# Optimization experiments

Measured on AMD Instinct MI355X. Metric: run time of the kernel, lower is better.

The kernel has to match this reference:

```python
import jax, jax.numpy as jnp
import numpy as np

N_NODES = 100000
N_EDGES = 1600000
HID = 128


def setup_inputs() -> dict:
    key = jax.random.key(0)
    ks = jax.random.split(key, 9)
    return {
        "x": jax.random.normal(ks[0], (N_NODES, 3), dtype=jnp.float32),
        "edge_index": jax.random.randint(ks[1], (2, N_EDGES), 0, N_NODES, dtype=jnp.int64),
        "W_lift": jax.random.normal(ks[2], (3, HID), dtype=jnp.float32) * 0.1,
        "b_lift": jax.random.normal(ks[3], (HID,), dtype=jnp.float32) * 0.1,
        "W_rel": jax.random.normal(ks[4], (HID, HID), dtype=jnp.float32) * 0.05,
        "b_rel": jax.random.normal(ks[5], (HID,), dtype=jnp.float32) * 0.05,
        "W_root": jax.random.normal(ks[6], (HID, HID), dtype=jnp.float32) * 0.05,
        "W_proj": jax.random.normal(ks[7], (HID, 1), dtype=jnp.float32) * 0.1,
        "b_proj": jax.random.normal(ks[8], (1,), dtype=jnp.float32) * 0.1,
    }


def reference(x, edge_index, W_lift, b_lift, W_rel, b_rel, W_root, W_proj, b_proj):
    # Lifting: [N, 3] -> [N, 128]
    h = x @ W_lift + b_lift
    # GraphConv (PyG): out_i = lin_rel(sum_{j in N(i)} h_j) + lin_root(h_i)
    src, dst = edge_index[0], edge_index[1]
    # gather neighbor features then scatter-add to targets
    agg = jax.ops.segment_sum(h[src], dst, num_segments=N_NODES)  # [N, 128]
    h = agg @ W_rel + b_rel + h @ W_root
    h = jnp.tanh(h)
    # Projection: [N, 128] -> [N, 1]
    return h @ W_proj + b_proj
```

## Files before the change

kernel.cpp:

```cpp
#include <hip/hip_runtime.h>
#include <stdint.h>

#define NN 100000
#define NE 1600000
#define HID 128

#define PSCALE 512.0f
#define PINV   (1.0f / 512.0f)
#define PBIAS  8.0f
#define FMASK  0x7FFFFULL

#define NBINS 391
#define CAP   5120
#define NB3   391
#define TB3   512
#define EB    4096

__device__ __forceinline__ void prep_weights(
    const float* __restrict__ W_lift, const float* __restrict__ b_lift,
    const float* __restrict__ W_rel, const float* __restrict__ b_rel,
    const float* __restrict__ W_root, float* __restrict__ Wf) {
    int t = threadIdx.x;
    if (t >= HID) return;
    float lr0 = 0.f, lr1 = 0.f, lr2 = 0.f;
    float xr0 = 0.f, xr1 = 0.f, xr2 = 0.f;
    float blr = 0.f, bxr = 0.f;
    for (int k = 0; k < HID; ++k) {
        float wr = W_rel[k * HID + t];
        float wo = W_root[k * HID + t];
        float bl = b_lift[k];
        float a0 = W_lift[0 * HID + k];
        float a1 = W_lift[1 * HID + k];
        float a2 = W_lift[2 * HID + k];
        lr0 += a0 * wr; lr1 += a1 * wr; lr2 += a2 * wr;
        xr0 += a0 * wo; xr1 += a1 * wo; xr2 += a2 * wo;
        blr += bl * wr; bxr += bl * wo;
    }
    Wf[0 * HID + t] = lr0;
    Wf[1 * HID + t] = lr1;
    Wf[2 * HID + t] = lr2;
    Wf[3 * HID + t] = xr0;
    Wf[4 * HID + t] = xr1;
    Wf[5 * HID + t] = xr2;
    Wf[6 * HID + t] = blr;
    Wf[7 * HID + t] = b_rel[t] + bxr;
}

__device__ __forceinline__ unsigned long long pack_edge(const float* __restrict__ x, int s) {
    float x0 = x[3 * s + 0];
    float x1 = x[3 * s + 1];
    float x2 = x[3 * s + 2];
    unsigned long long u0 = (unsigned)__float2int_rn((x0 + PBIAS) * PSCALE);
    unsigned long long u1 = (unsigned)__float2int_rn((x1 + PBIAS) * PSCALE);
    unsigned long long u2 = (unsigned)__float2int_rn((x2 + PBIAS) * PSCALE);
    return u0 | (u1 << 19) | (u2 << 38) | (1ULL << 57);
}

__global__ __launch_bounds__(TB3) void radix_scatter_prep(
    const int* __restrict__ edges,
    const float* __restrict__ x,
    unsigned* __restrict__ galloc,
    ulonglong2* __restrict__ records,
    const float* __restrict__ W_lift,
    const float* __restrict__ b_lift,
    const float* __restrict__ W_rel,
    const float* __restrict__ b_rel,
    const float* __restrict__ W_root,
    float* __restrict__ Wf) {
    if (blockIdx.x == NB3) {
        prep_weights(W_lift, b_lift, W_rel, b_rel, W_root, Wf);
        return;
    }
    __shared__ unsigned hist[NBINS];
    __shared__ unsigned base[NBINS];
    for (int j = threadIdx.x; j < NBINS; j += TB3) hist[j] = 0;
    __syncthreads();

    const int e0 = blockIdx.x * EB;
    for (int k = 0; k < EB; k += TB3) {
        int e = e0 + k + threadIdx.x;
        if (e >= NE) break;
        int d = edges[NE + e];
        if ((unsigned)d < NN) atomicAdd(&hist[d >> 8], 1u);
    }
    __syncthreads();
    for (int j = threadIdx.x; j < NBINS; j += TB3) {
        unsigned c = hist[j];
        base[j] = c ? atomicAdd(&galloc[j], c) : 0u;
        hist[j] = 0;
    }
    __syncthreads();
    for (int k = 0; k < EB; k += TB3) {
        int e = e0 + k + threadIdx.x;
        if (e >= NE) break;
        int s = edges[e];
        int d = edges[NE + e];
        if ((unsigned)s >= NN || (unsigned)d >= NN) continue;
        unsigned long long pk = pack_edge(x, s);
        int b = d >> 8;
        unsigned pos = base[b] + atomicAdd(&hist[b], 1u);
        if (pos < CAP)
            records[(size_t)b * CAP + pos] = make_ulonglong2((unsigned long long)d, pk);
    }
}

__global__ __launch_bounds__(256) void accum_node_kernel(
    const unsigned* __restrict__ galloc,
    const ulonglong2* __restrict__ records,
    const float* __restrict__ x,
    const float* __restrict__ Wf,
    const float* __restrict__ W_proj,
    const float* __restrict__ b_proj,
    float* __restrict__ out) {
    __shared__ unsigned long long acc[256];
    __shared__ float sWt[HID][8];
    __shared__ float sP[HID];
    acc[threadIdx.x] = 0ULL;
    for (int j = threadIdx.x; j < 8 * HID; j += blockDim.x) {
        int r = j >> 7;
        int t = j & (HID - 1);
        sWt[t][r] = Wf[j];
    }
    for (int j = threadIdx.x; j < HID; j += blockDim.x) sP[j] = W_proj[j];
    __syncthreads();

    const int b = blockIdx.x;
    unsigned cnt = galloc[b];
    if (cnt > CAP) cnt = CAP;
    const ulonglong2* rec = records + (size_t)b * CAP;
    for (unsigned i = threadIdx.x; i < cnt; i += 256) {
        ulonglong2 r = rec[i];
        atomicAdd(&acc[(unsigned)r.x & 255u], r.y);
    }
    __syncthreads();

    int node = b * 256 + threadIdx.x;
    if (node >= NN) return;

    unsigned long long p = acc[threadIdx.x];
    float degf = (float)(unsigned)(p >> 57);
    float a0 = (float)(unsigned)(p & FMASK) * PINV - PBIAS * degf;
    float a1 = (float)(unsigned)((p >> 19) & FMASK) * PINV - PBIAS * degf;
    float a2 = (float)(unsigned)((p >> 38) & FMASK) * PINV - PBIAS * degf;

    float x0 = x[3 * node + 0];
    float x1 = x[3 * node + 1];
    float x2 = x[3 * node + 2];

    float s = 0.f;
#pragma unroll 8
    for (int t = 0; t < HID; ++t) {
        float4 A = *(const float4*)&sWt[t][0];
        float4 B = *(const float4*)&sWt[t][4];
        float h = B.w
                + a0 * A.x + a1 * A.y + a2 * A.z
                + x0 * A.w + x1 * B.x + x2 * B.y
                + degf * B.z;
        float th = 1.f - 2.f / (__expf(2.f * h) + 1.f);
        s += th * sP[t];
    }
    out[node] = s + b_proj[0];
}

__global__ __launch_bounds__(256) void scatter_prep_kernel(
    const int* __restrict__ edges,
    const float* __restrict__ x,
    unsigned long long* __restrict__ aggp,
    const float* __restrict__ W_lift,
    const float* __restrict__ b_lift,
    const float* __restrict__ W_rel,
    const float* __restrict__ b_rel,
    const float* __restrict__ W_root,
    float* __restrict__ Wf) {
    if (blockIdx.x == 0) {
        prep_weights(W_lift, b_lift, W_rel, b_rel, W_root, Wf);
        return;
    }
    int e = (blockIdx.x - 1) * blockDim.x + threadIdx.x;
    if (e >= NE) return;
    int s = edges[e];
    int d = edges[NE + e];
    if ((unsigned)s >= NN || (unsigned)d >= NN) return;
    atomicAdd(&aggp[d], pack_edge(x, s));
}

__global__ __launch_bounds__(256) void node_kernel(
    const float* __restrict__ x,
    const unsigned long long* __restrict__ aggp,
    const float* __restrict__ Wf,
    const float* __restrict__ W_proj,
    const float* __restrict__ b_proj,
    float* __restrict__ out) {
    __shared__ float sWt[HID][8];
    __shared__ float sP[HID];
    for (int j = threadIdx.x; j < 8 * HID; j += blockDim.x) {
        int r = j >> 7;
        int t = j & (HID - 1);
        sWt[t][r] = Wf[j];
    }
    for (int j = threadIdx.x; j < HID; j += blockDim.x) sP[j] = W_proj[j];
    __syncthreads();

    int i = blockIdx.x * blockDim.x + threadIdx.x;
    if (i >= NN) return;

    unsigned long long p = aggp[i];
    float degf = (float)(unsigned)(p >> 57);
    float a0 = (float)(unsigned)(p & FMASK) * PINV - PBIAS * degf;
    float a1 = (float)(unsigned)((p >> 19) & FMASK) * PINV - PBIAS * degf;
    float a2 = (float)(unsigned)((p >> 38) & FMASK) * PINV - PBIAS * degf;

    float x0 = x[3 * i + 0];
    float x1 = x[3 * i + 1];
    float x2 = x[3 * i + 2];

    float acc = 0.f;
#pragma unroll 8
    for (int t = 0; t < HID; ++t) {
        float4 A = *(const float4*)&sWt[t][0];
        float4 B = *(const float4*)&sWt[t][4];
        float h = B.w
                + a0 * A.x + a1 * A.y + a2 * A.z
                + x0 * A.w + x1 * B.x + x2 * B.y
                + degf * B.z;
        float th = 1.f - 2.f / (__expf(2.f * h) + 1.f);
        acc += th * sP[t];
    }
    out[i] = acc + b_proj[0];
}

extern "C" void kernel_launch(void* const* d_in, const int* in_sizes, int n_in,
                              void* d_out, int out_size, void* d_ws, size_t ws_size,
                              hipStream_t stream) {
    const float* x      = (const float*)d_in[0];
    const int*   edges  = (const int*)d_in[1];
    const float* W_lift = (const float*)d_in[2];
    const float* b_lift = (const float*)d_in[3];
    const float* W_rel  = (const float*)d_in[4];
    const float* b_rel  = (const float*)d_in[5];
    const float* W_root = (const float*)d_in[6];
    const float* W_proj = (const float*)d_in[7];
    const float* b_proj = (const float*)d_in[8];
    float* out = (float*)d_out;

    const size_t off_rec = 4096;
    const size_t off_wf  = off_rec + (size_t)NBINS * CAP * 16;
    const size_t needed  = off_wf + 8 * HID * sizeof(float);

    if (ws_size >= needed) {
        unsigned* galloc = (unsigned*)d_ws;
        ulonglong2* records = (ulonglong2*)((char*)d_ws + off_rec);
        float* Wf = (float*)((char*)d_ws + off_wf);

        hipMemsetAsync(galloc, 0, NBINS * sizeof(unsigned), stream);
        radix_scatter_prep<<<NB3 + 1, TB3, 0, stream>>>(
            edges, x, galloc, records, W_lift, b_lift, W_rel, b_rel, W_root, Wf);
        accum_node_kernel<<<NBINS, 256, 0, stream>>>(
            galloc, records, x, Wf, W_proj, b_proj, out);
    } else {
        unsigned long long* aggp = (unsigned long long*)d_ws;
        float* Wf = (float*)((char*)d_ws + (size_t)NN * 8);
        hipMemsetAsync(aggp, 0, (size_t)NN * 8, stream);
        scatter_prep_kernel<<<1 + (NE + 255) / 256, 256, 0, stream>>>(
            edges, x, aggp, W_lift, b_lift, W_rel, b_rel, W_root, Wf);
        node_kernel<<<(NN + 255) / 256, 256, 0, stream>>>(
            x, aggp, Wf, W_proj, b_proj, out);
    }
}
```

Measured before the change: 145.8 us.

## Compact edge records to 8 bytes and shard bin allocators per XCD

Edge records shrink from 16 to 8 bytes by storing only the low destination byte and three 13-bit quantized coordinates, which are re-expanded into the packed accumulator format in the accumulate kernel. Each bin's global allocation counter and record region is split into eight slices indexed by the hardware XCC id, meant to cut cross-die atomic contention and keep record writes local. Edge indices are now loaded once into registers and reused across the histogram and scatter passes instead of being re-read. Clamping to 13 bits narrows the representable range, and each slice's capacity of 1280 risks overflow, which silently drops edges if XCC assignment is uneven.

```diff
diff --git a/kernel.cpp b/kernel.cpp
--- a/kernel.cpp
+++ b/kernel.cpp
@@ -11,10 +11,18 @@
 #define FMASK  0x7FFFFULL
 
 #define NBINS 391
-#define CAP   5120
+#define NSLC  8
+#define SCAP  1280
 #define NB3   391
 #define TB3   512
 #define EB    4096
+#define EPT   (EB / TB3)
+
+__device__ __forceinline__ unsigned xcc_id() {
+    unsigned x;
+    asm volatile("s_getreg_b32 %0, hwreg(HW_REG_XCC_ID)" : "=s"(x));
+    return x & (NSLC - 1);
+}
 
 __device__ __forceinline__ void prep_weights(
     const float* __restrict__ W_lift, const float* __restrict__ b_lift,
@@ -46,21 +54,11 @@
     Wf[7 * HID + t] = b_rel[t] + bxr;
 }
 
-__device__ __forceinline__ unsigned long long pack_edge(const float* __restrict__ x, int s) {
-    float x0 = x[3 * s + 0];
-    float x1 = x[3 * s + 1];
-    float x2 = x[3 * s + 2];
-    unsigned long long u0 = (unsigned)__float2int_rn((x0 + PBIAS) * PSCALE);
-    unsigned long long u1 = (unsigned)__float2int_rn((x1 + PBIAS) * PSCALE);
-    unsigned long long u2 = (unsigned)__float2int_rn((x2 + PBIAS) * PSCALE);
-    return u0 | (u1 << 19) | (u2 << 38) | (1ULL << 57);
-}
-
 __global__ __launch_bounds__(TB3) void radix_scatter_prep(
     const int* __restrict__ edges,
     const float* __restrict__ x,
     unsigned* __restrict__ galloc,
-    ulonglong2* __restrict__ records,
+    unsigned long long* __restrict__ records,
     const float* __restrict__ W_lift,
     const float* __restrict__ b_lift,
     const float* __restrict__ W_rel,
@@ -76,37 +74,52 @@
     for (int j = threadIdx.x; j < NBINS; j += TB3) hist[j] = 0;
     __syncthreads();
 
+    const unsigned myxcd = xcc_id();
     const int e0 = blockIdx.x * EB;
-    for (int k = 0; k < EB; k += TB3) {
-        int e = e0 + k + threadIdx.x;
-        if (e >= NE) break;
-        int d = edges[NE + e];
-        if ((unsigned)d < NN) atomicAdd(&hist[d >> 8], 1u);
+
+    int sreg[EPT], dreg[EPT];
+#pragma unroll
+    for (int k = 0; k < EPT; ++k) {
+        int e = e0 + k * TB3 + threadIdx.x;
+        int s = (e < NE) ? edges[e] : -1;
+        int d = (e < NE) ? edges[NE + e] : -1;
+        bool ok = ((unsigned)s < NN) && ((unsigned)d < NN);
+        sreg[k] = ok ? s : -1;
+        dreg[k] = ok ? d : -1;
+        if (ok) atomicAdd(&hist[d >> 8], 1u);
     }
     __syncthreads();
     for (int j = threadIdx.x; j < NBINS; j += TB3) {
         unsigned c = hist[j];
-        base[j] = c ? atomicAdd(&galloc[j], c) : 0u;
+        base[j] = c ? atomicAdd(&galloc[j * NSLC + myxcd], c) : 0u;
         hist[j] = 0;
     }
     __syncthreads();
-    for (int k = 0; k < EB; k += TB3) {
-        int e = e0 + k + threadIdx.x;
-        if (e >= NE) break;
-        int s = edges[e];
-        int d = edges[NE + e];
-        if ((unsigned)s >= NN || (unsigned)d >= NN) continue;
-        unsigned long long pk = pack_edge(x, s);
+#pragma unroll
+    for (int k = 0; k < EPT; ++k) {
+        int d = dreg[k];
+        if (d < 0) continue;
+        int s = sreg[k];
+        float x0 = x[3 * s + 0];
+        float x1 = x[3 * s + 1];
+        float x2 = x[3 * s + 2];
+        unsigned u0 = min((unsigned)__float2int_rn((x0 + PBIAS) * PSCALE), 8191u);
+        unsigned u1 = min((unsigned)__float2int_rn((x1 + PBIAS) * PSCALE), 8191u);
+        unsigned u2 = min((unsigned)__float2int_rn((x2 + PBIAS) * PSCALE), 8191u);
+        unsigned long long r = (unsigned long long)(d & 255)
+                             | ((unsigned long long)u0 << 8)
+                             | ((unsigned long long)u1 << 21)
+                             | ((unsigned long long)u2 << 34);
         int b = d >> 8;
         unsigned pos = base[b] + atomicAdd(&hist[b], 1u);
-        if (pos < CAP)
-            records[(size_t)b * CAP + pos] = make_ulonglong2((unsigned long long)d, pk);
+        if (pos < SCAP)
+            records[((size_t)b * NSLC + myxcd) * SCAP + pos] = r;
     }
 }
 
 __global__ __launch_bounds__(256) void accum_node_kernel(
     const unsigned* __restrict__ galloc,
-    const ulonglong2* __restrict__ records,
+    const unsigned long long* __restrict__ records,
     const float* __restrict__ x,
     const float* __restrict__ Wf,
     const float* __restrict__ W_proj,
@@ -125,12 +138,19 @@
     __syncthreads();
 
     const int b = blockIdx.x;
-    unsigned cnt = galloc[b];
-    if (cnt > CAP) cnt = CAP;
-    const ulonglong2* rec = records + (size_t)b * CAP;
-    for (unsigned i = threadIdx.x; i < cnt; i += 256) {
-        ulonglong2 r = rec[i];
-        atomicAdd(&acc[(unsigned)r.x & 255u], r.y);
+#pragma unroll
+    for (int sl = 0; sl < NSLC; ++sl) {
+        unsigned cnt = galloc[b * NSLC + sl];
+        if (cnt > SCAP) cnt = SCAP;
+        const unsigned long long* rec = records + ((size_t)b * NSLC + sl) * SCAP;
+        for (unsigned i = threadIdx.x; i < cnt; i += 256) {
+            unsigned long long r = rec[i];
+            unsigned long long add = ((r >> 8)  & 0x1FFFULL)
+                                   | (((r >> 21) & 0x1FFFULL) << 19)
+                                   | (((r >> 34) & 0x1FFFULL) << 38)
+                                   | (1ULL << 57);
+            atomicAdd(&acc[(unsigned)r & 255u], add);
+        }
     }
     __syncthreads();
 
@@ -181,7 +201,13 @@
     int s = edges[e];
     int d = edges[NE + e];
     if ((unsigned)s >= NN || (unsigned)d >= NN) return;
-    atomicAdd(&aggp[d], pack_edge(x, s));
+    float x0 = x[3 * s + 0];
+    float x1 = x[3 * s + 1];
+    float x2 = x[3 * s + 2];
+    unsigned long long u0 = (unsigned)__float2int_rn((x0 + PBIAS) * PSCALE);
+    unsigned long long u1 = (unsigned)__float2int_rn((x1 + PBIAS) * PSCALE);
+    unsigned long long u2 = (unsigned)__float2int_rn((x2 + PBIAS) * PSCALE);
+    atomicAdd(&aggp[d], u0 | (u1 << 19) | (u2 << 38) | (1ULL << 57));
 }
 
 __global__ __launch_bounds__(256) void node_kernel(
@@ -243,16 +269,16 @@
     const float* b_proj = (const float*)d_in[8];
     float* out = (float*)d_out;
 
-    const size_t off_rec = 4096;
-    const size_t off_wf  = off_rec + (size_t)NBINS * CAP * 16;
+    const size_t off_rec = 16384;
+    const size_t off_wf  = off_rec + (size_t)NBINS * NSLC * SCAP * 8;
     const size_t needed  = off_wf + 8 * HID * sizeof(float);
 
     if (ws_size >= needed) {
         unsigned* galloc = (unsigned*)d_ws;
-        ulonglong2* records = (ulonglong2*)((char*)d_ws + off_rec);
+        unsigned long long* records = (unsigned long long*)((char*)d_ws + off_rec);
         float* Wf = (float*)((char*)d_ws + off_wf);
 
-        hipMemsetAsync(galloc, 0, NBINS * sizeof(unsigned), stream);
+        hipMemsetAsync(galloc, 0, NBINS * NSLC * sizeof(unsigned), stream);
         radix_scatter_prep<<<NB3 + 1, TB3, 0, stream>>>(
             edges, x, galloc, records, W_lift, b_lift, W_rel, b_rel, W_root, Wf);
         accum_node_kernel<<<NBINS, 256, 0, stream>>>(
```

New measurement: 135.9 us. -6.8%, faster.
